# Kernel optimization log

Measured on AMD Instinct MI355X. Metric: run time of the kernel, lower is better.

## Reference

```python
import jax, jax.numpy as jnp
import numpy as np
from jax import lax

G = 64      # ngroup
CPN = 4     # channels per group in hidden layers
H, W = 32, 64
K = 5       # conv kernel
BIN = 8     # bin_num
BIAS = 3.5  # (bin_num-1)/2
NMIX = 3    # GMM components (batch replicas)
SCALE = 65536.0


def _group_mask(cout, cin, strict):
    # wavefront causality: tap (dg, di, dj) allowed iff dg+di+dj < 0 (strict) or <= 0
    g = jnp.arange(G)
    dg = g[None, :] - g[:, None]                      # (Gout, Gin)
    off = jnp.arange(K) - K // 2
    dd = off[:, None] + off[None, :]                  # (K, K)
    tot = dg[:, :, None, None] + dd[None, None, :, :]
    m = (tot < 0) if strict else (tot <= 0)
    m = jnp.repeat(jnp.repeat(m, cout, axis=0), cin, axis=1)
    return m.astype(jnp.float32)                      # (G*cout, G*cin, K, K)


def _cconv(x, w, b, m, relu):
    y = lax.conv_general_dilated(x, w * m, (1, 1), 'SAME',
                                 dimension_numbers=('NCHW', 'OIHW', 'NCHW'))
    y = y + b[None, :, None, None]
    return jax.nn.relu(y) if relu else y


def setup_inputs() -> dict:
    key = jax.random.key(0)
    ks = jax.random.split(key, 8)
    data = jax.random.randint(ks[0], (1, G, H, W), 0, BIN).astype(jnp.float32)
    mask = jax.random.randint(ks[1], (1, G, H, W), 0, 2).astype(jnp.float32)
    s = 0.05
    w_in = jax.random.normal(ks[2], (G * CPN, G, K, K), jnp.float32) * s
    b_in = jnp.zeros((G * CPN,), jnp.float32)
    w_hid = jax.random.normal(ks[3], (10, G * CPN, G * CPN, K, K), jnp.float32) * s
    b_hid = jnp.zeros((10, G * CPN), jnp.float32)
    w_out = jax.random.normal(ks[4], (G * NMIX, G * CPN, K, K), jnp.float32) * s
    b_out = jnp.zeros((G * NMIX,), jnp.float32)
    return dict(data=data, mask=mask, w_in=w_in, b_in=b_in,
                w_hid=w_hid, b_hid=b_hid, w_out=w_out, b_out=b_out)


def reference(data, mask, w_in, b_in, w_hid, b_hid, w_out, b_out):
    m_in = _group_mask(CPN, 1, True)      # first layer: strict (excludes current group)
    m_hid = _group_mask(CPN, CPN, False)
    m_out = _group_mask(NMIX, CPN, False)
    tdata = (data - BIAS) * mask
    x = jnp.concatenate([tdata, tdata, tdata], axis=0)   # (3, G, H, W)
    x = _cconv(x, w_in, b_in, m_in, True)
    for i in range(5):                                   # 5 residual blocks
        h = _cconv(x, w_hid[2 * i], b_hid[2 * i], m_hid, True)
        h = _cconv(h, w_hid[2 * i + 1], b_hid[2 * i + 1], m_hid, True)
        x = x + h
    y = _cconv(x, w_out, b_out, m_out, False)            # (3, G*3, H, W)
    y = y.reshape(NMIX, G, NMIX, H, W)                   # batch replica m -> mixture m
    logits = y[:, :, 0]
    mu = y[:, :, 1]
    sig = jax.nn.softplus(y[:, :, 2]) + 1e-6
    wts = jax.nn.softmax(logits, axis=0)                 # (3, G, H, W)
    edges = jnp.arange(BIN, dtype=jnp.float32) + 0.5 - BIAS
    z = (edges[:, None, None, None, None] - mu[None]) / (sig[None] * jnp.float32(np.sqrt(2.0)))
    cdf = 0.5 * (1.0 + lax.erf(z))                       # (BIN, 3, G, H, W)
    table = jnp.einsum('kmghw,mghw->ghwk', cdf, wts) * SCALE
    return table                                         # (G, H, W, BIN) quantizable CDF
```

## Files before the change

### kernel.cpp

```cpp
#include <hip/hip_runtime.h>
#include <math.h>

typedef _Float16 f16;
typedef _Float16 f16x8 __attribute__((ext_vector_type(8)));
typedef float f32x4 __attribute__((ext_vector_type(4)));

#define HH 32
#define WW 64
#define NPX 2048
#define SLOTS 68
#define CHS 78336
#define LOSCALE 2048.0f
#define INV_LOSCALE 4.8828125e-4f

typedef const __attribute__((address_space(1))) void gvoid;
typedef __attribute__((address_space(3))) void lvoid;
__device__ __forceinline__ void gload_lds16(const void* g, void* l) {
    __builtin_amdgcn_global_load_lds((gvoid*)g, (lvoid*)l, 16, 0, 0);
}

__global__ void zero_kernel(f16* p, int n8) {
    int i = blockIdx.x * 256 + threadIdx.x;
    if (i < n8) *(int4*)(p + i * 8) = make_int4(0, 0, 0, 0);
}

__global__ void prep_kernel(const float* __restrict__ data,
                            const float* __restrict__ mask,
                            f16* __restrict__ X0, int plane) {
    int idx = blockIdx.x * 256 + threadIdx.x;
    if (idx >= NPX * 64) return;
    int px = idx >> 6, ci = idx & 63;
    int hh = px >> 6, w = px & 63;
    float v = (data[ci * NPX + px] - 3.5f) * mask[ci * NPX + px];
    int dst = (ci >> 5) * CHS + ((hh + 2) * SLOTS + (w + 2)) * 32 + (ci & 31);
    X0[dst] = (f16)v;
    X0[plane + dst] = (f16)0.f;
}

__global__ void repack_kernel(const float* __restrict__ W, f16* __restrict__ WP,
                              int cin_log2, int coutp_log2,
                              int cpg_in_log2, int limb, int is_out) {
    int idx = blockIdx.x * 256 + threadIdx.x;
    int Cin = 1 << cin_log2;
    int plane = 25 << (cin_log2 + coutp_log2);
    int ci = idx & (Cin - 1);
    int rest = idx >> cin_log2;
    int co_p = rest & ((1 << coutp_log2) - 1);
    int tap = rest >> coutp_log2;
    if (tap >= 25) return;
    int ky = tap / 5, kx = tap - 5 * ky;
    int co_orig, g_out;
    if (is_out) { g_out = co_p >> 1; co_orig = 3 * g_out + 1 + (co_p & 1); }
    else        { g_out = co_p >> 2; co_orig = co_p; }
    int g_in = ci >> cpg_in_log2;
    float v = 0.f;
    if (ky + kx <= limb + g_out - g_in)
        v = W[(co_orig * Cin + ci) * 25 + tap];
    f16 vh = (f16)v;
    int dst = (((tap << (coutp_log2 - 4)) + (co_p >> 4)) << (cin_log2 - 5 + 9))
            + ((ci >> 5) << 9) + ((co_p & 15) << 5) + (ci & 31);
    WP[dst] = vh;
    WP[plane + dst] = (f16)((v - (float)vh) * LOSCALE);
}

__global__ __launch_bounds__(320, 3) void conv_kernel(
    const f16* __restrict__ IN, int Cin, int inPlane,
    const f16* __restrict__ WP, int wPlane,
    const float* __restrict__ bias,
    const f16* __restrict__ RES, int resPlane,
    f16* __restrict__ OA, int oaPlane,
    float* __restrict__ OT,
    int nmt, int Coutp, int cpg_out, int cpg_in, int limb, int mode)
{
    __shared__ __align__(16) char SMEM[46080];
    f16* BL = (f16*)SMEM;
    float* RED = (float*)SMEM;

    const int t = threadIdx.x;
    const int kw = t >> 6;
    const int lane = t & 63, l15 = lane & 15, q = lane >> 4;

    const int b = blockIdx.x;
    const int p3 = b & 7, r = b >> 3;
    int pairIdx, slot, h_;
    if (nmt == 16) { pairIdx = p3;     h_ = r & 31; slot = r >> 5; }
    else           { pairIdx = p3 & 3; h_ = r;      slot = p3 >> 2; }
    const int h = h_;
    const int mt = slot ? (nmt - 1 - pairIdx) : pairIdx;
    const int co0 = mt * 16;
    const int g_max = (co0 + 15) / cpg_out;

    int cnt[5];
#pragma unroll
    for (int kx = 0; kx < 5; kx++) {
        int c = (g_max + limb - (kw + kx) + 1) * cpg_in;
        c = c < Cin ? c : Cin;
        cnt[kx] = c > 0 ? c : 0;
    }
    int ci_top = (g_max + limb + 1) * cpg_in;
    ci_top = ci_top < Cin ? ci_top : Cin;

    const f16* src[9];
#pragma unroll
    for (int rr = 0; rr < 9; rr++) {
        int u = rr * 320 + t;
        if (u >= 2720) u = 0;
        int pl = u >= 1360 ? 1 : 0;
        int rem = u - pl * 1360;
        src[rr] = IN + (size_t)pl * inPlane + h * 2176 + rem * 8;
    }

    f32x4 acc_h[4], acc_m[4];
#pragma unroll
    for (int j = 0; j < 4; j++) {
        acc_h[j] = (f32x4){0.f, 0.f, 0.f, 0.f};
        acc_m[j] = (f32x4){0.f, 0.f, 0.f, 0.f};
    }

    const size_t kxs = (size_t)Coutp * Cin;
    const f16* wb0 = WP + (size_t)(kw * 5 * (Coutp >> 4) + mt) * ((size_t)Cin << 4)
                   + l15 * 32 + q * 8;

    int coff = 0;
    for (int ci0 = 0; ci0 < ci_top; ci0 += 32, coff += CHS) {
        __syncthreads();
#pragma unroll
        for (int rr = 0; rr < 9; rr++) {
            int ub = rr * 320 + kw * 64;
            if (ub < 2720)
                gload_lds16(src[rr] + coff, BL + ub * 8);
        }
        const f16* wb = wb0 + (ci0 >> 5) * 512;
        f16x8 cah, cal, nah, nal;
        if (ci0 < cnt[0]) {
            cah = *(const f16x8*)(wb);
            cal = *(const f16x8*)(wb + wPlane);
        }
        __syncthreads();

#pragma unroll
        for (int kx = 0; kx < 5; kx++) {
            if (ci0 >= cnt[kx]) break;
            if (kx < 4 && ci0 < cnt[kx + 1]) {
                nah = *(const f16x8*)(wb + (kx + 1) * kxs);
                nal = *(const f16x8*)(wb + (kx + 1) * kxs + wPlane);
            }
            f16x8 bh[4], bl[4];
#pragma unroll
            for (int j = 0; j < 4; j++) {
                int slt = j * 16 + l15 + kx;
                bh[j] = *(const f16x8*)&BL[(0 * 5 + kw) * (SLOTS * 32) + slt * 32 + q * 8];
                bl[j] = *(const f16x8*)&BL[(1 * 5 + kw) * (SLOTS * 32) + slt * 32 + q * 8];
            }
#pragma unroll
            for (int j = 0; j < 4; j++) {
                acc_h[j] = __builtin_amdgcn_mfma_f32_16x16x32_f16(cah, bh[j], acc_h[j], 0, 0, 0);
                acc_m[j] = __builtin_amdgcn_mfma_f32_16x16x32_f16(cah, bl[j], acc_m[j], 0, 0, 0);
                acc_m[j] = __builtin_amdgcn_mfma_f32_16x16x32_f16(cal, bh[j], acc_m[j], 0, 0, 0);
            }
            cah = nah; cal = nal;
        }
    }

    __syncthreads();
#pragma unroll
    for (int j = 0; j < 4; j++) {
        f32x4 v;
#pragma unroll
        for (int rr = 0; rr < 4; rr++)
            v[rr] = acc_h[j][rr] + acc_m[j][rr] * INV_LOSCALE;
        *(f32x4*)&RED[(kw * 64 + j * 16 + l15) * 20 + q * 4] = v;
    }
    __syncthreads();

    if (mode == 0) {
        for (int c = t; c < 1024; c += 320) {
            int px = c >> 4, col = c & 15;
            float v = bias[co0 + col];
#pragma unroll
            for (int k5 = 0; k5 < 5; k5++) v += RED[(k5 * 64 + px) * 20 + col];
            v = fmaxf(v, 0.f);
            int cc = co0 + col;
            int o = (cc >> 5) * CHS + ((h + 2) * SLOTS + px + 2) * 32 + (cc & 31);
            if (RES) v += (float)RES[o] + (float)RES[resPlane + o] * INV_LOSCALE;
            f16 vh = (f16)v;
            OA[o] = vh;
            OA[oaPlane + o] = (f16)((v - (float)vh) * LOSCALE);
        }
    } else {
        for (int c = t; c < 1024; c += 320) {
            int px = c >> 4, col = c & 15;
            float v = bias[3 * ((co0 + col) >> 1) + 1 + (col & 1)];
#pragma unroll
            for (int k5 = 0; k5 < 5; k5++) v += RED[(k5 * 64 + px) * 20 + col];
            RED[px * 20 + col] = v;
        }
        __syncthreads();
        for (int c = t; c < 512; c += 320) {
            int px = c >> 3, gl = c & 7;
            float mu = RED[px * 20 + 2 * gl];
            float s  = RED[px * 20 + 2 * gl + 1];
            float sp = fmaxf(s, 0.f) + log1pf(expf(-fabsf(s)));
            float sig = sp + 1e-6f;
            float inv = 1.f / (sig * 1.41421356237f);
            int g = (co0 >> 1) + gl;
            float* o = OT + ((size_t)g * NPX + h * WW + px) * 8;
#pragma unroll
            for (int k = 0; k < 8; k++) {
                float z = ((float)k - 3.0f - mu) * inv;
                o[k] = 32768.f * (1.f + erff(z));
            }
        }
    }
}

extern "C" void kernel_launch(void* const* d_in, const int* in_sizes, int n_in,
                              void* d_out, int out_size, void* d_ws, size_t ws_size,
                              hipStream_t stream) {
    const float* data  = (const float*)d_in[0];
    const float* mask  = (const float*)d_in[1];
    const float* w_in  = (const float*)d_in[2];
    const float* b_in  = (const float*)d_in[3];
    const float* w_hid = (const float*)d_in[4];
    const float* b_hid = (const float*)d_in[5];
    const float* w_out = (const float*)d_in[6];
    const float* b_out = (const float*)d_in[7];
    float* out = (float*)d_out;

    f16* WP = (f16*)d_ws;
    f16* P  = WP + 3276800;
    f16* Q  = P + 1253376;
    f16* X0 = Q + 1253376;

    zero_kernel<<<1377, 256, 0, stream>>>(P, 352512);
    prep_kernel<<<512, 256, 0, stream>>>(data, mask, X0, 156672);

    repack_kernel<<<1600, 256, 0, stream>>>(w_in, WP, 6, 8, 0, 3, 0);
    conv_kernel<<<512, 320, 0, stream>>>(X0, 64, 156672, WP, 409600,
        b_in, nullptr, 0, P, 626688, nullptr, 16, 256, 4, 1, 3, 0);

    for (int i = 0; i < 5; i++) {
        repack_kernel<<<6400, 256, 0, stream>>>(w_hid + (size_t)(2 * i) * 1638400,
                                                WP, 8, 8, 2, 4, 0);
        conv_kernel<<<512, 320, 0, stream>>>(P, 256, 626688, WP, 1638400,
            b_hid + 2 * i * 256, nullptr, 0, Q, 626688, nullptr, 16, 256, 4, 4, 4, 0);
        repack_kernel<<<6400, 256, 0, stream>>>(w_hid + (size_t)(2 * i + 1) * 1638400,
                                                WP, 8, 8, 2, 4, 0);
        conv_kernel<<<512, 320, 0, stream>>>(Q, 256, 626688, WP, 1638400,
            b_hid + (2 * i + 1) * 256, P, 626688, P, 626688, nullptr, 16, 256, 4, 4, 4, 0);
    }

    repack_kernel<<<3200, 256, 0, stream>>>(w_out, WP, 8, 7, 2, 4, 1);
    conv_kernel<<<256, 320, 0, stream>>>(P, 256, 626688, WP, 819200,
        b_out, nullptr, 0, nullptr, 0, out, 8, 128, 2, 4, 4, 1);
}
```

Measured before the change: 448.7 us.

## Overlap next-layer weight repack with current conv via extra blocks and double buffering

Removes the separate zero, prep and repack launches. Zeroing, input prep and the first repack go into one init kernel. Each later layer's weight repack now runs as extra trailing blocks of the previous conv launch and writes into a second, double-buffered weight workspace. Repack is restructured as a tiled, LDS-staged transpose with float4 loads. This cuts launch count and hides repack time behind conv work, at the cost of more shared memory (51200 bytes), which may lower conv occupancy, and a doubled weight workspace.

```diff
diff --git a/kernel.cpp b/kernel.cpp
--- a/kernel.cpp
+++ b/kernel.cpp
@@ -19,48 +19,65 @@
     __builtin_amdgcn_global_load_lds((gvoid*)g, (lvoid*)l, 16, 0, 0);
 }
 
-__global__ void zero_kernel(f16* p, int n8) {
-    int i = blockIdx.x * 256 + threadIdx.x;
-    if (i < n8) *(int4*)(p + i * 8) = make_int4(0, 0, 0, 0);
-}
-
-__global__ void prep_kernel(const float* __restrict__ data,
-                            const float* __restrict__ mask,
-                            f16* __restrict__ X0, int plane) {
-    int idx = blockIdx.x * 256 + threadIdx.x;
-    if (idx >= NPX * 64) return;
-    int px = idx >> 6, ci = idx & 63;
-    int hh = px >> 6, w = px & 63;
-    float v = (data[ci * NPX + px] - 3.5f) * mask[ci * NPX + px];
-    int dst = (ci >> 5) * CHS + ((hh + 2) * SLOTS + (w + 2)) * 32 + (ci & 31);
-    X0[dst] = (f16)v;
-    X0[plane + dst] = (f16)0.f;
-}
-
-__global__ void repack_kernel(const float* __restrict__ W, f16* __restrict__ WP,
-                              int cin_log2, int coutp_log2,
-                              int cpg_in_log2, int limb, int is_out) {
-    int idx = blockIdx.x * 256 + threadIdx.x;
-    int Cin = 1 << cin_log2;
-    int plane = 25 << (cin_log2 + coutp_log2);
-    int ci = idx & (Cin - 1);
-    int rest = idx >> cin_log2;
-    int co_p = rest & ((1 << coutp_log2) - 1);
-    int tap = rest >> coutp_log2;
-    if (tap >= 25) return;
-    int ky = tap / 5, kx = tap - 5 * ky;
-    int co_orig, g_out;
-    if (is_out) { g_out = co_p >> 1; co_orig = 3 * g_out + 1 + (co_p & 1); }
-    else        { g_out = co_p >> 2; co_orig = co_p; }
-    int g_in = ci >> cpg_in_log2;
-    float v = 0.f;
-    if (ky + kx <= limb + g_out - g_in)
-        v = W[(co_orig * Cin + ci) * 25 + tap];
-    f16 vh = (f16)v;
-    int dst = (((tap << (coutp_log2 - 4)) + (co_p >> 4)) << (cin_log2 - 5 + 9))
-            + ((ci >> 5) << 9) + ((co_p & 15) << 5) + (ci & 31);
-    WP[dst] = vh;
-    WP[plane + dst] = (f16)((v - (float)vh) * LOSCALE);
+__device__ __forceinline__ void repack_tile(
+    const float* __restrict__ W, f16* __restrict__ WP, float* RAWF,
+    int Cin, int nCoT, int nCic, int cpg_in_log2, int limb, int is_out,
+    int coT, int cic, int plane)
+{
+    const int nt = blockDim.x, t = threadIdx.x;
+    const int co0 = coT * 16, ci0 = cic * 32;
+    for (int u = t; u < 3200; u += nt) {
+        int co16 = u / 200, j4 = u - co16 * 200;
+        int co_p = co0 + co16;
+        int co_orig = is_out ? 3 * (co_p >> 1) + 1 + (co_p & 1) : co_p;
+        float4 v = *(const float4*)(W + (size_t)(co_orig * Cin + ci0) * 25 + j4 * 4);
+        *(float4*)&RAWF[co16 * 800 + j4 * 4] = v;
+    }
+    __syncthreads();
+    const int base = (coT * nCic + cic) * 512;
+    const int tapStride = nCoT * nCic * 512;
+    for (int e = t; e < 12800; e += nt) {
+        int tap = e >> 9, r = e & 511;
+        int co16 = r >> 5, ci32 = r & 31;
+        int ky = tap / 5, kx = tap - 5 * ky;
+        int co_p = co0 + co16;
+        int g_out = is_out ? (co_p >> 1) : (co_p >> 2);
+        int g_in = (ci0 + ci32) >> cpg_in_log2;
+        float v = 0.f;
+        if (ky + kx <= limb + g_out - g_in)
+            v = RAWF[co16 * 800 + ci32 * 25 + tap];
+        f16 vh = (f16)v;
+        int dst = base + tap * tapStride + co16 * 32 + ci32;
+        WP[dst] = vh;
+        WP[plane + dst] = (f16)((v - (float)vh) * LOSCALE);
+    }
+}
+
+__global__ __launch_bounds__(256) void init_kernel(
+    const float* __restrict__ data, const float* __restrict__ mask,
+    f16* __restrict__ PQ, f16* __restrict__ X0,
+    const float* __restrict__ w_in, f16* __restrict__ WP)
+{
+    __shared__ __align__(16) float RAWF[12800];
+    const int b = blockIdx.x, t = threadIdx.x;
+    if (b < 1224) {
+        *(int4*)(PQ + (size_t)(b * 256 + t) * 8) = make_int4(0, 0, 0, 0);
+    } else if (b < 1836) {
+        int e = (b - 1224) * 256 + t;
+        int si = e >> 6, ci = e & 63;
+        int row = si / 68, slot = si - row * 68;
+        float v = 0.f;
+        if (row >= 2 && row < 34 && slot >= 2 && slot < 66) {
+            int px = (row - 2) * 64 + (slot - 2);
+            v = (data[ci * NPX + px] - 3.5f) * mask[ci * NPX + px];
+        }
+        int dst = (ci >> 5) * CHS + si * 32 + (ci & 31);
+        X0[dst] = (f16)v;
+        X0[156672 + dst] = (f16)0.f;
+    } else {
+        int rb = b - 1836;
+        repack_tile(w_in, WP, RAWF, 64, 16, 2, 0, 3, 0, rb >> 1, rb & 1, 409600);
+    }
 }
 
 __global__ __launch_bounds__(320, 3) void conv_kernel(
@@ -70,11 +87,21 @@
     const f16* __restrict__ RES, int resPlane,
     f16* __restrict__ OA, int oaPlane,
     float* __restrict__ OT,
-    int nmt, int Coutp, int cpg_out, int cpg_in, int limb, int mode)
+    int nmt, int Coutp, int cpg_out, int cpg_in, int limb, int mode,
+    const float* __restrict__ rW, f16* __restrict__ rWP,
+    int rCin, int rnCoT, int rnCic, int rcpg_in_log2, int rlimb, int ris_out,
+    int rplane, int nConv)
 {
-    __shared__ __align__(16) char SMEM[46080];
+    __shared__ __align__(16) char SMEM[51200];
     f16* BL = (f16*)SMEM;
     float* RED = (float*)SMEM;
+
+    if (blockIdx.x >= (unsigned)nConv) {
+        int rb = blockIdx.x - nConv;
+        repack_tile(rW, rWP, (float*)SMEM, rCin, rnCoT, rnCic,
+                    rcpg_in_log2, rlimb, ris_out, rb / rnCic, rb % rnCic, rplane);
+        return;
+    }
 
     const int t = threadIdx.x;
     const int kw = t >> 6;
@@ -227,30 +254,43 @@
     const float* b_out = (const float*)d_in[7];
     float* out = (float*)d_out;
 
-    f16* WP = (f16*)d_ws;
-    f16* P  = WP + 3276800;
-    f16* Q  = P + 1253376;
-    f16* X0 = Q + 1253376;
-
-    zero_kernel<<<1377, 256, 0, stream>>>(P, 352512);
-    prep_kernel<<<512, 256, 0, stream>>>(data, mask, X0, 156672);
-
-    repack_kernel<<<1600, 256, 0, stream>>>(w_in, WP, 6, 8, 0, 3, 0);
-    conv_kernel<<<512, 320, 0, stream>>>(X0, 64, 156672, WP, 409600,
-        b_in, nullptr, 0, P, 626688, nullptr, 16, 256, 4, 1, 3, 0);
-
-    for (int i = 0; i < 5; i++) {
-        repack_kernel<<<6400, 256, 0, stream>>>(w_hid + (size_t)(2 * i) * 1638400,
-                                                WP, 8, 8, 2, 4, 0);
-        conv_kernel<<<512, 320, 0, stream>>>(P, 256, 626688, WP, 1638400,
-            b_hid + 2 * i * 256, nullptr, 0, Q, 626688, nullptr, 16, 256, 4, 4, 4, 0);
-        repack_kernel<<<6400, 256, 0, stream>>>(w_hid + (size_t)(2 * i + 1) * 1638400,
-                                                WP, 8, 8, 2, 4, 0);
-        conv_kernel<<<512, 320, 0, stream>>>(Q, 256, 626688, WP, 1638400,
-            b_hid + (2 * i + 1) * 256, P, 626688, P, 626688, nullptr, 16, 256, 4, 4, 4, 0);
-    }
-
-    repack_kernel<<<3200, 256, 0, stream>>>(w_out, WP, 8, 7, 2, 4, 1);
-    conv_kernel<<<256, 320, 0, stream>>>(P, 256, 626688, WP, 819200,
-        b_out, nullptr, 0, nullptr, 0, out, 8, 128, 2, 4, 4, 1);
-}
+    f16* WPA = (f16*)d_ws;
+    f16* WPB = WPA + 3276800;
+    f16* P   = WPB + 3276800;
+    f16* Q   = P + 1253376;
+    f16* X0  = Q + 1253376;
+
+    init_kernel<<<1868, 256, 0, stream>>>(data, mask, P, X0, w_in, WPA);
+
+    f16* cur = WPA;
+    f16* nxt = WPB;
+
+    conv_kernel<<<640, 320, 0, stream>>>(X0, 64, 156672, cur, 409600,
+        b_in, nullptr, 0, P, 626688, nullptr, 16, 256, 4, 1, 3, 0,
+        w_hid, nxt, 256, 16, 8, 2, 4, 0, 1638400, 512);
+    { f16* tmp = cur; cur = nxt; nxt = tmp; }
+
+    for (int k = 1; k <= 10; ++k) {
+        const int isLast = (k == 10);
+        const float* rw = isLast ? w_out : (w_hid + (size_t)k * 1638400);
+        const int rgrid = isLast ? 64 : 128;
+        const int rnCoT = isLast ? 8 : 16;
+        const int ris   = isLast ? 1 : 0;
+        const int rpl   = isLast ? 819200 : 1638400;
+        if (k & 1)
+            conv_kernel<<<512 + rgrid, 320, 0, stream>>>(P, 256, 626688, cur, 1638400,
+                b_hid + (size_t)(k - 1) * 256, nullptr, 0, Q, 626688, nullptr,
+                16, 256, 4, 4, 4, 0,
+                rw, nxt, 256, rnCoT, 8, 2, 4, ris, rpl, 512);
+        else
+            conv_kernel<<<512 + rgrid, 320, 0, stream>>>(Q, 256, 626688, cur, 1638400,
+                b_hid + (size_t)(k - 1) * 256, P, 626688, P, 626688, nullptr,
+                16, 256, 4, 4, 4, 0,
+                rw, nxt, 256, rnCoT, 8, 2, 4, ris, rpl, 512);
+        f16* tmp = cur; cur = nxt; nxt = tmp;
+    }
+
+    conv_kernel<<<256, 320, 0, stream>>>(P, 256, 626688, cur, 819200,
+        b_out, nullptr, 0, nullptr, 0, out, 8, 128, 2, 4, 4, 1,
+        nullptr, nullptr, 256, 8, 1, 2, 4, 0, 0, 256);
+}
```

New measurement: 450.5 us. Within noise of the previous version (+0.4%).
